# Kernel tuning notes

Measured on AMD Instinct MI355X. Metric: run time of the kernel, lower is better.

The kernel has to match this reference:

```python
import jax, jax.numpy as jnp
import numpy as np

B, N, C_IN, C_EMB, G = 16, 1024, 16, 64, 128
NEG = -1e12


def _lap(m):
    # m @ D^-1/2, transpose, @ D^-1/2  (matches torch code incl. transpose)
    d = jnp.sum(m, axis=1) ** -0.5
    return (m * d[None, :]).T * d[None, :]


def setup_inputs():
    key = jax.random.key(0)
    ks = jax.random.split(key, 16)
    f = jax.random.normal
    return {
        'x': f(ks[0], (B, C_IN, N), jnp.float32),
        'ct': f(ks[1], (B, C_EMB, N), jnp.float32),
        'graph_data': jax.random.uniform(ks[2], (2, N, N), dtype=jnp.float32),
        'emb_w': f(ks[3], (C_EMB, C_IN)) / np.sqrt(C_IN).astype(np.float32),
        'emb_b': f(ks[4], (C_EMB,)) * 0.01,
        'emb2_w': f(ks[5], (N, N)) / np.sqrt(N).astype(np.float32),
        'emb2_b': f(ks[6], (N,)) * 0.01,
        'att_W': f(ks[7], (C_EMB, C_EMB)) / np.sqrt(C_EMB).astype(np.float32),
        'att_a': f(ks[8], (2 * C_EMB, 1)) / np.sqrt(2 * C_EMB).astype(np.float32),
        'att_GL': f(ks[9], (N, G)) / np.sqrt(G).astype(np.float32),
        'uai_w': f(ks[10], (C_EMB, C_EMB)) / np.sqrt(C_EMB).astype(np.float32),
        'uai_b': f(ks[11], (C_EMB,)) * 0.01,
        'lin1_w': f(ks[12], (C_EMB, C_EMB)) / np.sqrt(C_EMB).astype(np.float32),
        'lin2_w': f(ks[13], (C_EMB, C_EMB)) / np.sqrt(C_EMB).astype(np.float32),
        'lin2_b': f(ks[14], (C_EMB,)) * 0.01,
        'ln_w': jnp.ones((C_EMB, N), jnp.float32),
        'ln_b': jnp.zeros((C_EMB, N), jnp.float32),
    }


def reference(x, ct, graph_data, emb_w, emb_b, emb2_w, emb2_b, att_W, att_a,
              att_GL, uai_w, uai_b, lin1_w, lin2_w, lin2_b, ln_w, ln_b):
    # emb: Conv1d k=1 -> leaky_relu -> Linear over node axis N
    h0 = jax.nn.leaky_relu(jnp.einsum('bcn,ec->ben', x, emb_w) + emb_b[None, :, None])
    h0 = jnp.einsum('ben,mn->bem', h0, emb2_w) + emb2_b[None, None, :]
    inp = jnp.swapaxes(h0, 1, 2)  # [B,N,C']

    # InterpositionAttention (repeat/cat factorized: e_ij = leakyrelu(a1.h_i + a2.h_j))
    eye = jnp.eye(N, dtype=x.dtype)
    adj_att = jax.nn.softmax(jax.nn.relu(att_GL @ att_GL.T), axis=-1) + eye
    h = inp @ att_W  # [B,N,C']
    e = jax.nn.leaky_relu((h @ att_a[:C_EMB]) + jnp.swapaxes(h @ att_a[C_EMB:], 1, 2))  # [B,N,N]
    att = jax.nn.softmax(jnp.where(adj_att > 0, e, NEG), axis=2)
    x_att = jnp.swapaxes(jax.nn.relu(att @ h), 1, 2)  # [B,C',N]

    # UAI module (eval mode: dropout off -> all MC samples equal -> sigma = 0)
    mu = jnp.swapaxes(x_att, 1, 2) @ uai_w.T + uai_b  # [B,N,C']
    x_uai = jnp.swapaxes(mu, 1, 2)  # [B,C',N]

    g1 = _lap(graph_data[0] + eye)
    g2 = _lap(graph_data[1] + eye)

    # learned adjacency from pairwise squared distances (cdist p=2, squared)
    xf = jnp.swapaxes(x_uai, 1, 2)  # [B,N,C']
    sq = jnp.sum(xf * xf, axis=-1)
    d2 = jnp.maximum(sq[:, :, None] + sq[:, None, :] - 2.0 * (xf @ jnp.swapaxes(xf, 1, 2)), 0.0)
    gl = jax.nn.softmax(jnp.exp(-d2 / (2.0 * C_EMB)) + eye, axis=-1)  # sigma^2 = emb_size

    def ln(z):  # LayerNorm over last two dims [C', N]
        m = jnp.mean(z, axis=(1, 2), keepdims=True)
        v = jnp.var(z, axis=(1, 2), keepdims=True)
        return (z - m) / jnp.sqrt(v + 1e-5) * ln_w + ln_b

    l1 = lambda z: jnp.einsum('oc,bcn->bon', lin1_w, z)
    l2 = lambda z: jnp.einsum('oc,bcn->bon', lin2_w, z) + lin2_b[None, :, None]

    x_new = ln(l1(x_uai) @ gl + l1(l1(x_uai) @ g1) @ g2)
    ft = jax.nn.gelu(ln(l2(x_uai) @ gl + l2(l2(x_uai) @ g1) @ g2), approximate=False)
    rt = ft  # rt is computed by the identical expression (dropout off)

    ct_new = ft * ct + x_new - ft * x_new
    ht = rt * jax.nn.elu(ct_new) + x_uai - rt * x_uai
    return (ht, ct_new)
```

## Files before the change

kernel.cpp:

```cpp
#include <hip/hip_runtime.h>
#include <math.h>

typedef unsigned short u16;
typedef __attribute__((ext_vector_type(8))) short short8;
typedef __attribute__((ext_vector_type(4))) float floatx4;

constexpr int BATCH = 16;
constexpr int NI = 1024;
constexpr int CE = 64;
constexpr int CI = 16;
constexpr long long NN2  = (long long)NI * NI;
constexpr long long BCN  = (long long)BATCH * CE * NI;
constexpr long long BNv  = (long long)BATCH * NI;
constexpr long long BNN  = (long long)BATCH * NI * NI;
constexpr long long S1 = (long long)CE * NI;
constexpr long long S2 = 2 * S1;

__device__ __forceinline__ float lrelu01(float x) { return x > 0.f ? x : 0.01f * x; }

__device__ __forceinline__ u16 f2bf(float f) {
  unsigned u = __builtin_bit_cast(unsigned, f);
  return (u16)((u + 0x7fffu + ((u >> 16) & 1u)) >> 16);
}
__device__ __forceinline__ float bf2f(u16 h) {
  unsigned u = ((unsigned)h) << 16;
  return __builtin_bit_cast(float, u);
}
__device__ __forceinline__ unsigned fkey(float f) {
  unsigned u = __builtin_bit_cast(unsigned, f);
  return (u & 0x80000000u) ? ~u : (u | 0x80000000u);
}
__device__ __forceinline__ float funkey(unsigned k) {
  unsigned u = (k & 0x80000000u) ? (k & 0x7fffffffu) : ~k;
  return __builtin_bit_cast(float, u);
}

template<int BM, int BN, int MODE>
__global__ __launch_bounds__(256) void mgemm(
    const u16* __restrict__ Ag, const u16* __restrict__ B1g, const u16* __restrict__ B2g,
    int K1, int K, int lda, int ldb, long long bsA, long long bsB1,
    float* __restrict__ Cf, u16* __restrict__ Cb, int ldc, long long bsC,
    const float* __restrict__ aux1, const float* __restrict__ aux2,
    const float* __restrict__ aux3, const float* __restrict__ aux4,
    float* __restrict__ Zout)
{
  constexpr int RM = BM / 2, RN = BN / 2, MI = RM / 16, NJ = RN / 16;
  __shared__ __align__(16) u16 As[BM * 64];
  __shared__ __align__(16) u16 Bs[BN * 64];
  __shared__ __align__(16) u16 xa[MODE == 13 ? 32 * 72 : 1];
  const int z = blockIdx.z;
  const int n0 = blockIdx.x * BN;
  const int r0 = blockIdx.y * BM;
  const u16* Ab = Ag + (long long)z * bsA + (long long)r0 * lda;
  const u16* Bb1 = B1g + (long long)z * bsB1 + (long long)n0 * ldb;
  const int tid = threadIdx.x;
  const int lane = tid & 63;
  const int wid = tid >> 6;
  const int wr = wid >> 1, wc = wid & 1;
  const int q = lane >> 4, mlow = lane & 15;

  floatx4 acc[MI][NJ] = {};
  float zp[(BM * 8) / 256] = {};

  for (int k0 = 0; k0 < K; k0 += 64) {
    if constexpr (MODE == 13) {
      const float* s1z = aux2 + (long long)z * NI;
      const float* s2z = aux3 + (long long)z * NI;
      const float mb = funkey(((const unsigned*)aux4)[z]);
#pragma unroll
      for (int s = 0; s < (BM * 8) / 256; s++) {
        int cid = tid + s * 256;
        int r = cid >> 3, craw = cid & 7;
        float s1r = s1z[r0 + r];
        float mr = lrelu01(s1r + mb);
        const float* sp = s2z + k0 + craw * 8;
        float4 sa = *(const float4*)sp;
        float4 sb = *(const float4*)(sp + 4);
        float p0 = __expf(lrelu01(s1r + sa.x) - mr);
        float p1 = __expf(lrelu01(s1r + sa.y) - mr);
        float p2 = __expf(lrelu01(s1r + sa.z) - mr);
        float p3 = __expf(lrelu01(s1r + sa.w) - mr);
        float p4 = __expf(lrelu01(s1r + sb.x) - mr);
        float p5 = __expf(lrelu01(s1r + sb.y) - mr);
        float p6 = __expf(lrelu01(s1r + sb.z) - mr);
        float p7 = __expf(lrelu01(s1r + sb.w) - mr);
        zp[s] += p0 + p1 + p2 + p3 + p4 + p5 + p6 + p7;
        uint4 v;
        v.x = (unsigned)f2bf(p0) | ((unsigned)f2bf(p1) << 16);
        v.y = (unsigned)f2bf(p2) | ((unsigned)f2bf(p3) << 16);
        v.z = (unsigned)f2bf(p4) | ((unsigned)f2bf(p5) << 16);
        v.w = (unsigned)f2bf(p6) | ((unsigned)f2bf(p7) << 16);
        *(uint4*)&As[(r * 8 + (craw ^ (r & 7))) * 8] = v;
      }
    } else {
      const u16* Asrc = Ab + k0;
#pragma unroll
      for (int s = 0; s < (BM * 8) / 256; s++) {
        int cid = tid + s * 256;
        int r = cid >> 3, craw = cid & 7;
        uint4 v = *(const uint4*)(Asrc + (long long)r * lda + craw * 8);
        *(uint4*)&As[(r * 8 + (craw ^ (r & 7))) * 8] = v;
      }
    }
    {
      const u16* Bsrc = (k0 < K1) ? (Bb1 + k0)
                                  : (B2g + (long long)n0 * ldb + (k0 - K1));
#pragma unroll
      for (int s = 0; s < (BN * 8) / 256; s++) {
        int cid = tid + s * 256;
        int r = cid >> 3, craw = cid & 7;
        uint4 v = *(const uint4*)(Bsrc + (long long)r * ldb + craw * 8);
        *(uint4*)&Bs[(r * 8 + (craw ^ (r & 7))) * 8] = v;
      }
    }
    __syncthreads();
#pragma unroll
    for (int kh = 0; kh < 2; kh++) {
      const int kc = kh * 4 + q;
      short8 afr[MI], bfr[NJ];
#pragma unroll
      for (int i = 0; i < MI; i++) {
        int row = wr * RM + i * 16 + mlow;
        afr[i] = *(const short8*)&As[(row * 8 + (kc ^ (row & 7))) * 8];
      }
#pragma unroll
      for (int j = 0; j < NJ; j++) {
        int row = wc * RN + j * 16 + mlow;
        bfr[j] = *(const short8*)&Bs[(row * 8 + (kc ^ (row & 7))) * 8];
      }
#pragma unroll
      for (int i = 0; i < MI; i++)
#pragma unroll
        for (int j = 0; j < NJ; j++)
          acc[i][j] = __builtin_amdgcn_mfma_f32_16x16x32_bf16(afr[i], bfr[j], acc[i][j], 0, 0, 0);
    }
    __syncthreads();
  }

  if constexpr (MODE == 3) {
    const float* sqb = aux1 + (long long)z * NI;
#pragma unroll
    for (int i = 0; i < MI; i++) {
#pragma unroll
      for (int rg = 0; rg < 4; rg++) {
        int r = r0 + wr * RM + i * 16 + q * 4 + rg;
        float sqi = sqb[r];
        float rsum = 0.f;
#pragma unroll
        for (int j = 0; j < NJ; j++) {
          int ncol = n0 + wc * RN + j * 16 + mlow;
          float d2 = fmaxf(sqi + sqb[ncol] - 2.f * acc[i][j][rg], 0.f);
          float w = __expf(__expf(-d2 * (1.f / 128.f)) + (r == ncol ? 1.f : 0.f) - 2.f);
          Cb[(long long)z * bsC + (long long)r * ldc + ncol] = f2bf(w);
          rsum += w;
        }
        rsum += __shfl_xor(rsum, 1);
        rsum += __shfl_xor(rsum, 2);
        rsum += __shfl_xor(rsum, 4);
        rsum += __shfl_xor(rsum, 8);
        if (mlow == 0) atomicAdd(&Zout[(long long)z * NI + r], rsum);
      }
    }
  } else if constexpr (MODE == 11) {
    float* sred = (float*)As;
#pragma unroll
    for (int i = 0; i < MI; i++) {
#pragma unroll
      for (int rg = 0; rg < 4; rg++) {
        int rloc = wr * RM + i * 16 + q * 4 + rg;
        int r = r0 + rloc;
        float rb = aux3[r];
        float ps1 = 0.f, ps2 = 0.f;
#pragma unroll
        for (int j = 0; j < NJ; j++) {
          int ncol = n0 + wc * RN + j * 16 + mlow;
          float v = acc[i][j][rg] + rb;
          Cb[(long long)z * bsC + (long long)r * ldc + ncol] = f2bf(v);
          ps1 = fmaf(v, aux1[ncol], ps1);
          ps2 = fmaf(v, aux2[ncol], ps2);
        }
        ps1 += __shfl_xor(ps1, 1); ps1 += __shfl_xor(ps1, 2);
        ps1 += __shfl_xor(ps1, 4); ps1 += __shfl_xor(ps1, 8);
        ps2 += __shfl_xor(ps2, 1); ps2 += __shfl_xor(ps2, 2);
        ps2 += __shfl_xor(ps2, 4); ps2 += __shfl_xor(ps2, 8);
        if (mlow == 0) { sred[rloc * 2 + wc] = ps1; sred[128 + rloc * 2 + wc] = ps2; }
      }
    }
    __syncthreads();
    if (tid < 64) {
      float v1 = sred[tid * 2] + sred[tid * 2 + 1];
      float v2 = sred[128 + tid * 2] + sred[128 + tid * 2 + 1];
      Cf[(long long)z * NI + r0 + tid] = v1;
      Zout[(long long)z * NI + r0 + tid] = v2;
      float mx = v2;
      for (int off = 1; off < 64; off <<= 1) mx = fmaxf(mx, __shfl_xor(mx, off));
      if (tid == 0) atomicMax((unsigned*)B2g + z, fkey(mx));
    }
  } else if constexpr (MODE == 13) {
    float* zred = (float*)xa;
    float* zinv = (float*)xa + 256;
    zred[(tid >> 3) * 8 + (tid & 7)] = zp[0];
    __syncthreads();
    if (tid < 32) {
      float sum = 0.f;
#pragma unroll
      for (int j = 0; j < 8; j++) sum += zred[tid * 8 + j];
      zinv[tid] = 1.f / sum;
    }
    __syncthreads();
    float zr[4];
#pragma unroll
    for (int rg = 0; rg < 4; rg++) zr[rg] = zinv[wr * 16 + q * 4 + rg];
    __syncthreads();
#pragma unroll
    for (int j = 0; j < NJ; j++) {
#pragma unroll
      for (int rg = 0; rg < 4; rg++) {
        int row = wr * 16 + q * 4 + rg;
        int col = wc * RN + j * 16 + mlow;
        float v = fmaxf(acc[0][j][rg] * zr[rg], 0.f);
        xa[row * 72 + col] = f2bf(v);
      }
    }
#pragma unroll
    for (int s = 0; s < 2; s++) {
      int cid = tid + s * 256;
      int r = cid >> 3, craw = cid & 7;
      *(uint4*)&Bs[(r * 8 + (craw ^ (r & 7))) * 8] =
          *(const uint4*)(B2g + r * 64 + craw * 8);
    }
    __syncthreads();
    floatx4 acc2[2] = {};
#pragma unroll
    for (int kh = 0; kh < 2; kh++) {
      const int kc = kh * 4 + q;
      short8 a2 = *(const short8*)&xa[(wr * 16 + mlow) * 72 + kc * 8];
#pragma unroll
      for (int j = 0; j < 2; j++) {
        int orow = wc * 32 + j * 16 + mlow;
        short8 b2 = *(const short8*)&Bs[(orow * 8 + (kc ^ (orow & 7))) * 8];
        acc2[j] = __builtin_amdgcn_mfma_f32_16x16x32_bf16(a2, b2, acc2[j], 0, 0, 0);
      }
    }
#pragma unroll
    for (int rg = 0; rg < 4; rg++) {
      int row = r0 + wr * 16 + q * 4 + rg;
      float sqp = 0.f;
#pragma unroll
      for (int j = 0; j < 2; j++) {
        int o = wc * 32 + j * 16 + mlow;
        float v = acc2[j][rg] + aux1[o];
        Cb[(long long)z * bsC + (long long)row * ldc + o] = f2bf(v);
        sqp = fmaf(v, v, sqp);
      }
      sqp += __shfl_xor(sqp, 1);
      sqp += __shfl_xor(sqp, 2);
      sqp += __shfl_xor(sqp, 4);
      sqp += __shfl_xor(sqp, 8);
      if (mlow == 0) atomicAdd(&Zout[(long long)z * NI + row], sqp);
    }
  } else if constexpr (MODE == 5) {
    float ts = 0.f, tss = 0.f;
#pragma unroll
    for (int i = 0; i < MI; i++) {
#pragma unroll
      for (int j = 0; j < NJ; j++) {
#pragma unroll
        for (int rg = 0; rg < 4; rg++) {
          int r = r0 + wr * RM + i * 16 + q * 4 + rg;
          int ncol = n0 + wc * RN + j * 16 + mlow;
          float v = acc[i][j][rg];
          v += aux3[r] * aux1[(long long)z * NI + ncol] + aux4[r] * aux2[ncol];
          Cf[(long long)z * bsC + (long long)r * ldc + ncol] = v;
          ts += v;
          tss = fmaf(v, v, tss);
        }
      }
    }
    float* red = (float*)As;
    red[tid] = ts; red[256 + tid] = tss;
    __syncthreads();
    for (int st = 128; st > 0; st >>= 1) {
      if (tid < st) { red[tid] += red[tid + st]; red[256 + tid] += red[256 + tid + st]; }
      __syncthreads();
    }
    if (tid == 0) {
      const int half = r0 >> 6;
      atomicAdd(&Zout[z * 2 + half], red[0]);
      atomicAdd(&Zout[32 + z * 2 + half], red[256]);
    }
  } else {
#pragma unroll
    for (int i = 0; i < MI; i++) {
#pragma unroll
      for (int j = 0; j < NJ; j++) {
#pragma unroll
        for (int rg = 0; rg < 4; rg++) {
          int r = r0 + wr * RM + i * 16 + q * 4 + rg;
          int ncol = n0 + wc * RN + j * 16 + mlow;
          float v = acc[i][j][rg];
          if constexpr (MODE == 4) {
            int blk = r >> 6, oo = r & 63;
            int drow = ((blk & 1) << 6) + oo;
            if (blk < 2) v = v / aux1[(long long)z * NI + ncol];
            Cb[(long long)z * bsC + (long long)drow * 2048 + (long long)(blk >> 1) * 1024 + ncol] =
                f2bf(v);
          } else {
            Cb[(long long)z * bsC + (long long)r * ldc + ncol] = f2bf(v);
          }
        }
      }
    }
  }
}

__global__ __launch_bounds__(256) void lap_rowsum(const float* __restrict__ gd,
                                                  float* __restrict__ dr)
{
  const int ki = blockIdx.x;
  const float* row = gd + (long long)ki * NI;
  float s = 0.f;
  for (int j = threadIdx.x; j < NI; j += 256) s += row[j];
  __shared__ float red[256];
  red[threadIdx.x] = s; __syncthreads();
  for (int st = 128; st > 0; st >>= 1) {
    if (threadIdx.x < st) red[threadIdx.x] += red[threadIdx.x + st];
    __syncthreads();
  }
  if (threadIdx.x == 0) dr[ki] = rsqrtf(red[0] + 1.f);
}

__global__ __launch_bounds__(256) void mega_prep(
    const float* __restrict__ l1w, const float* __restrict__ l2w,
    const float* __restrict__ l2b, const float* __restrict__ uaiw,
    const float* __restrict__ attW, const float* __restrict__ atta,
    u16* __restrict__ stack4, float* __restrict__ rb2ext, float* __restrict__ rl2ext,
    u16* __restrict__ uaiw_bf, u16* __restrict__ attwT_bf, float* __restrict__ w12,
    const float* __restrict__ emb2w, u16* __restrict__ emb2w_bf,
    const float* __restrict__ x, const float* __restrict__ ew,
    const float* __restrict__ eb, u16* __restrict__ h0a,
    const float* __restrict__ gd, const float* __restrict__ dsum,
    u16* __restrict__ g2t, u16* __restrict__ g1,
    float* __restrict__ cs1)
{
  __shared__ float sm[1088];
  const int bid = blockIdx.x;
  const int t = threadIdx.x;
  if (bid < 98) {
    const int gid = bid * 256 + t;
    if (gid < 4096) {
      stack4[gid] = f2bf(l1w[gid]);
    } else if (gid < 8192) {
      stack4[gid] = f2bf(l2w[gid - 4096]);
    } else if (gid < 12288) {
      int tt = gid - 8192, o = tt >> 6, m = tt & 63;
      float s = 0.f;
      for (int c = 0; c < 64; c++) s = fmaf(l1w[o * 64 + c], l1w[c * 64 + m], s);
      stack4[gid] = f2bf(s);
    } else if (gid < 16384) {
      int tt = gid - 12288, o = tt >> 6, m = tt & 63;
      float s = 0.f;
      for (int c = 0; c < 64; c++) s = fmaf(l2w[o * 64 + c], l2w[c * 64 + m], s);
      stack4[gid] = f2bf(s);
    } else if (gid < 16512) {
      int r = gid - 16384;
      rb2ext[r] = (r < 64) ? 0.f : l2b[r - 64];
    } else if (gid < 16640) {
      int r = gid - 16512;
      float v = 0.f;
      if (r >= 64) { int o = r - 64; for (int c = 0; c < 64; c++) v = fmaf(l2w[o * 64 + c], l2b[c], v); }
      rl2ext[r] = v;
    } else if (gid < 20736) {
      uaiw_bf[gid - 16640] = f2bf(uaiw[gid - 16640]);
    } else if (gid < 24832) {
      int idx = gid - 20736;
      int k = idx >> 6, e = idx & 63;
      attwT_bf[idx] = f2bf(attW[e * 64 + k]);
    } else if (gid < 24960) {
      int c = gid - 24832;
      int cc = c & 63, which = c >> 6;
      float s = 0.f;
      for (int k = 0; k < 64; k++) s = fmaf(attW[cc * 64 + k], atta[which * 64 + k], s);
      w12[c] = s;
    }
  } else if (bid < 4194) {
    const long long i = (long long)(bid - 98) * 256 + t;
    emb2w_bf[i] = f2bf(emb2w[i]);
  } else if (bid < 5218) {
    const int be = bid - 4194;
    const int b = be >> 6, e = be & 63;
    float* w = sm;
    if (t < CI) w[t] = ew[e * CI + t];
    __syncthreads();
    const float bias = eb[e];
    const float* xb = x + (long long)b * CI * NI;
    u16* outp = h0a + (long long)be * NI;
    for (int n = t; n < NI; n += 256) {
      float a = bias;
#pragma unroll
      for (int c = 0; c < CI; c++) a = fmaf(xb[c * NI + n], w[c], a);
      outp[n] = f2bf(lrelu01(a));
    }
  } else if (bid < 9314) {
    const long long idx = (long long)(bid - 5218) * 256 + t;
    const int m = (int)(idx >> 10), j = (int)(idx & 1023);
    const float* d = dsum + NI;
    float v = (gd[NN2 + idx] + (m == j ? 1.f : 0.f)) * d[m] * d[j];
    g2t[idx] = f2bf(v);
  } else if (bid < 10338) {
    const int sub = bid - 9314;
    const int bx = (sub & 31) * 32, by = (sub >> 5) * 32;
    const int lx = t & 31, ly = t >> 5;
    float* tile = sm;
    for (int yy = ly; yy < 32; yy += 8)
      tile[yy * 33 + lx] = gd[(long long)(by + yy) * NI + bx + lx];
    __syncthreads();
    for (int yy = ly; yy < 32; yy += 8) {
      const int i = bx + yy, j = by + lx;
      float v = (tile[lx * 33 + yy] + (i == j ? 1.f : 0.f)) * dsum[i] * dsum[j];
      g1[(long long)i * NI + j] = f2bf(v);
    }
  } else {
    const int n = bid - 10338;
    float s = 0.f;
    for (int i = t; i < NI; i += 256) s = fmaf(gd[(long long)n * NI + i], dsum[i], s);
    float* red = sm;
    red[t] = s; __syncthreads();
    for (int st = 128; st > 0; st >>= 1) {
      if (t < st) red[t] += red[t + st];
      __syncthreads();
    }
    if (t == 0) cs1[n] = dsum[n] * (red[0] + dsum[n]);
  }
}

__global__ __launch_bounds__(256) void csv2_kernel(const float* __restrict__ gd1,
                                                   const float* __restrict__ d,
                                                   const float* __restrict__ cs1,
                                                   float* __restrict__ cs2,
                                                   float* __restrict__ v2)
{
  const int m = blockIdx.x;
  float s = 0.f, sv = 0.f;
  for (int n = threadIdx.x; n < NI; n += 256) {
    float g = gd1[(long long)m * NI + n] * d[n];
    s += g;
    sv = fmaf(g, cs1[n], sv);
  }
  __shared__ float r1[256], r2[256];
  r1[threadIdx.x] = s; r2[threadIdx.x] = sv; __syncthreads();
  for (int st = 128; st > 0; st >>= 1) {
    if (threadIdx.x < st) { r1[threadIdx.x] += r1[threadIdx.x + st]; r2[threadIdx.x] += r2[threadIdx.x + st]; }
    __syncthreads();
  }
  if (threadIdx.x == 0) {
    cs2[m] = d[m] * (r1[0] + d[m]);
    v2[m] = d[m] * (r2[0] + d[m] * cs1[m]);
  }
}

__global__ __launch_bounds__(256) void cc_kernel(const u16* __restrict__ W,
                                                 const float* __restrict__ Zgl,
                                                 const float* __restrict__ cs2,
                                                 float* __restrict__ cc)
{
  const int b = blockIdx.y;
  const int wid = threadIdx.x >> 6, lane = threadIdx.x & 63;
  const int m = blockIdx.x * 4 + wid;
  const u16* row = W + (long long)b * NN2 + (long long)m * NI;
  const float* zz = Zgl + (long long)b * NI;
  float s = 0.f;
#pragma unroll
  for (int it = 0; it < 4; it++) {
    const int j0 = it * 256 + lane * 4;
    uint2 pk = *(const uint2*)(row + j0);
    float4 zv = *(const float4*)(zz + j0);
    s += bf2f((u16)(pk.x & 0xffff)) / zv.x + bf2f((u16)(pk.x >> 16)) / zv.y
       + bf2f((u16)(pk.y & 0xffff)) / zv.z + bf2f((u16)(pk.y >> 16)) / zv.w;
  }
  for (int off = 1; off < 64; off <<= 1) s += __shfl_xor(s, off);
  if (lane == 0) cc[(long long)b * NI + m] = s + cs2[m];
}

__global__ __launch_bounds__(256) void ln_final_t(const float* __restrict__ T,
                                                  const float* __restrict__ stats,
                                                  const float* __restrict__ lnw,
                                                  const float* __restrict__ lnb,
                                                  const float* __restrict__ ct,
                                                  const u16* __restrict__ xuT,
                                                  float* __restrict__ outp)
{
  __shared__ float xs[64 * 65];
  const int blk = blockIdx.x;
  const int b = blk >> 4;
  const int n0 = (blk & 15) << 6;
  const int t = threadIdx.x;
  const int tc = t & 63, tr = t >> 6;
#pragma unroll
  for (int i = 0; i < 16; i++) {
    int nn = i * 4 + tr;
    xs[tc * 65 + nn] = bf2f(xuT[((long long)b << 16) + (long long)(n0 + nn) * 64 + tc]);
  }
  __syncthreads();
  const float inv_n = 1.f / 65536.f;
  const float m0 = stats[b * 2] * inv_n;
  const float m1 = stats[b * 2 + 1] * inv_n;
  const float rs0 = rsqrtf(fmaxf(stats[32 + b * 2] * inv_n - m0 * m0, 0.f) + 1e-5f);
  const float rs1 = rsqrtf(fmaxf(stats[32 + b * 2 + 1] * inv_n - m1 * m1, 0.f) + 1e-5f);
#pragma unroll
  for (int j = 0; j < 16; j++) {
    const int c = j * 4 + tr;
    const int n = n0 + tc;
    const int rem = c * NI + n;
    const long long toff = (long long)b * S2 + rem;
    const float t0 = T[toff];
    const float t1 = T[toff + S1];
    const float w = lnw[rem], bb = lnb[rem];
    const float xn = (t0 - m0) * rs0 * w + bb;
    float ft = (t1 - m1) * rs1 * w + bb;
    ft = 0.5f * ft * (1.f + erff(ft * 0.70710678118654752f));
    const float u = xs[c * 65 + tc];
    const long long oidx = ((long long)b << 16) + rem;
    const float cn = fmaf(ft, ct[oidx] - xn, xn);
    const float el = cn > 0.f ? cn : expm1f(cn);
    outp[oidx] = fmaf(ft, el - u, u);
    outp[BCN + oidx] = cn;
  }
}

extern "C" void kernel_launch(void* const* d_in, const int* in_sizes, int n_in,
                              void* d_out, int out_size, void* d_ws, size_t ws_size,
                              hipStream_t stream)
{
  (void)in_sizes; (void)n_in; (void)out_size; (void)ws_size;
  const float* x      = (const float*)d_in[0];
  const float* ct     = (const float*)d_in[1];
  const float* gdata  = (const float*)d_in[2];
  const float* emb_w  = (const float*)d_in[3];
  const float* emb_b  = (const float*)d_in[4];
  const float* emb2_w = (const float*)d_in[5];
  const float* emb2_b = (const float*)d_in[6];
  const float* att_W  = (const float*)d_in[7];
  const float* att_a  = (const float*)d_in[8];
  const float* uai_w  = (const float*)d_in[10];
  const float* uai_b  = (const float*)d_in[11];
  const float* lin1_w = (const float*)d_in[12];
  const float* lin2_w = (const float*)d_in[13];
  const float* lin2_b = (const float*)d_in[14];
  const float* ln_w   = (const float*)d_in[15];
  const float* ln_b   = (const float*)d_in[16];
  float* outp = (float*)d_out;

  float* ws = (float*)d_ws;
  long long o = 0;
  auto af = [&](long long n) { float* p = ws + o; o += (n + 63) & ~63LL; return p; };
  auto au = [&](long long n) { return (u16*)af((n + 1) / 2); };

  float* Tacc    = af(S2 * BATCH);
  float* s1      = af(BNv);
  float* s2      = af(BNv);
  float* dsum    = af(2 * NI);
  float* cs1v    = af(NI);
  float* cs2v    = af(NI);
  float* v2v     = af(NI);
  float* ccv     = af(BNv);
  float* rb2ext  = af(128);
  float* rl2ext  = af(128);
  float* w12     = af(128);
  float* zeroreg = af(2 * BNv + 80);
  float* Zgl     = zeroreg;
  float* sqv     = zeroreg + BNv;
  float* stats   = zeroreg + 2 * BNv;
  unsigned* s2mU = (unsigned*)(stats + 64);
  u16* emb2w_bf  = au(NN2);
  u16* h0a_bf    = au(S1 * BATCH);
  u16* h0Tb      = au(S1 * BATCH);
  u16* hTb       = au(S1 * BATCH);
  u16* xuaiTb    = au(S1 * BATCH);
  u16* g1b       = au(NN2);
  u16* g2tb      = au(NN2);
  u16* G12b      = au(NN2);
  u16* Abig      = au((long long)BATCH * 128 * 2048);
  u16* stack4    = au(256 * 64);
  u16* uaiw_bf   = au(CE * CE);
  u16* attwT_bf  = au(CE * CE);
  u16* bigW      = au(BNN);

  hipMemsetAsync(zeroreg, 0, (2 * BNv + 80) * sizeof(float), stream);

  lap_rowsum<<<2 * NI, 256, 0, stream>>>(gdata, dsum);

  mega_prep<<<11362, 256, 0, stream>>>(
      lin1_w, lin2_w, lin2_b, uai_w, att_W, att_a,
      stack4, rb2ext, rl2ext, uaiw_bf, attwT_bf, w12,
      emb2_w, emb2w_bf, x, emb_w, emb_b, h0a_bf,
      gdata, dsum, g2tb, g1b, cs1v);

  csv2_kernel<<<NI, 256, 0, stream>>>(gdata + NN2, dsum + NI, cs1v, cs2v, v2v);

  mgemm<64, 64, 6><<<dim3(16, 16, 1), 256, 0, stream>>>(
      g2tb, g1b, nullptr, NI, NI, NI, NI, 0, 0,
      nullptr, G12b, NI, 0, nullptr, nullptr, nullptr, nullptr, nullptr);

  mgemm<64, 64, 11><<<dim3(1, 16, BATCH), 256, 0, stream>>>(
      emb2w_bf, h0a_bf, (const u16*)s2mU, NI, NI, NI, NI, 0, S1,
      s1, h0Tb, CE, S1, w12, w12 + 64, emb2_b, nullptr, s2);

  mgemm<64, 64, 6><<<dim3(16, 1, BATCH), 256, 0, stream>>>(
      attwT_bf, h0Tb, nullptr, CE, CE, CE, CE, 0, S1,
      nullptr, hTb, NI, S1, nullptr, nullptr, nullptr, nullptr, nullptr);

  mgemm<32, 64, 13><<<dim3(1, 32, BATCH), 256, 0, stream>>>(
      hTb, hTb, uaiw_bf, NI, NI, NI, NI, 0, S1,
      nullptr, xuaiTb, CE, S1, uai_b, s1, s2, (const float*)s2mU, sqv);

  mgemm<128, 128, 3><<<dim3(8, 8, BATCH), 256, 0, stream>>>(
      xuaiTb, xuaiTb, nullptr, CE, CE, CE, CE, S1, S1,
      nullptr, bigW, NI, NN2, sqv, nullptr, nullptr, nullptr, Zgl);

  cc_kernel<<<dim3(NI / 4, BATCH), 256, 0, stream>>>(bigW, Zgl, cs2v, ccv);

  mgemm<64, 64, 4><<<dim3(16, 4, BATCH), 256, 0, stream>>>(
      stack4, xuaiTb, nullptr, CE, CE, CE, CE, 0, S1,
      nullptr, Abig, 0, (long long)128 * 2048, Zgl, nullptr, nullptr, nullptr, nullptr);

  mgemm<64, 64, 5><<<dim3(16, 2, BATCH), 256, 0, stream>>>(
      Abig, bigW, G12b, NI, 2 * NI, 2048, NI, (long long)128 * 2048, NN2,
      Tacc, nullptr, NI, S2, ccv, v2v, rb2ext, rl2ext, stats);

  ln_final_t<<<256, 256, 0, stream>>>(Tacc, stats, ln_w, ln_b, ct, xuaiTb, outp);
}
```

Baseline: 257.2 us.

## Reassociate embedding and attention-weight GEMMs, emit transposed conv output directly

The attention weight is now applied to the small conv-1d output before the large node-axis Linear, so the big N x N GEMM produces h directly. A new epilogue mode folds the Linear bias through the column sums of the attention weight and computes the attention logit projections from att_a. The conv-1d prep now writes its output transposed with vectorized stores, and the G12 GEMM tile shape changes. This removes the intermediate h0T round trip. The new epilogue's reduction and indexing must match the old semantics exactly.

Result: no change. 259.3 us (+0.8%).

```diff
diff --git a/kernel.cpp b/kernel.cpp
--- a/kernel.cpp
+++ b/kernel.cpp
@@ -161,39 +161,33 @@
         if (mlow == 0) atomicAdd(&Zout[(long long)z * NI + r], rsum);
       }
     }
-  } else if constexpr (MODE == 11) {
+  } else if constexpr (MODE == 14) {
+    float ps1 = 0.f, ps2 = 0.f;
+#pragma unroll
+    for (int i = 0; i < MI; i++) {
+#pragma unroll
+      for (int rg = 0; rg < 4; rg++) {
+        int r = wr * RM + i * 16 + q * 4 + rg;
+        int ncol = n0 + wc * RN + mlow;
+        float v = acc[i][0][rg] + aux3[r] * aux1[ncol];
+        Cb[(long long)z * bsC + (long long)r * ldc + ncol] = f2bf(v);
+        ps1 = fmaf(v, aux2[r], ps1);
+        ps2 = fmaf(v, aux2[64 + r], ps2);
+      }
+    }
+    ps1 += __shfl_xor(ps1, 16); ps1 += __shfl_xor(ps1, 32);
+    ps2 += __shfl_xor(ps2, 16); ps2 += __shfl_xor(ps2, 32);
     float* sred = (float*)As;
-#pragma unroll
-    for (int i = 0; i < MI; i++) {
-#pragma unroll
-      for (int rg = 0; rg < 4; rg++) {
-        int rloc = wr * RM + i * 16 + q * 4 + rg;
-        int r = r0 + rloc;
-        float rb = aux3[r];
-        float ps1 = 0.f, ps2 = 0.f;
-#pragma unroll
-        for (int j = 0; j < NJ; j++) {
-          int ncol = n0 + wc * RN + j * 16 + mlow;
-          float v = acc[i][j][rg] + rb;
-          Cb[(long long)z * bsC + (long long)r * ldc + ncol] = f2bf(v);
-          ps1 = fmaf(v, aux1[ncol], ps1);
-          ps2 = fmaf(v, aux2[ncol], ps2);
-        }
-        ps1 += __shfl_xor(ps1, 1); ps1 += __shfl_xor(ps1, 2);
-        ps1 += __shfl_xor(ps1, 4); ps1 += __shfl_xor(ps1, 8);
-        ps2 += __shfl_xor(ps2, 1); ps2 += __shfl_xor(ps2, 2);
-        ps2 += __shfl_xor(ps2, 4); ps2 += __shfl_xor(ps2, 8);
-        if (mlow == 0) { sred[rloc * 2 + wc] = ps1; sred[128 + rloc * 2 + wc] = ps2; }
-      }
-    }
-    __syncthreads();
-    if (tid < 64) {
+    const int col = wc * RN + mlow;
+    if (q == 0) { sred[col * 2 + wr] = ps1; sred[64 + col * 2 + wr] = ps2; }
+    __syncthreads();
+    if (tid < 32) {
       float v1 = sred[tid * 2] + sred[tid * 2 + 1];
-      float v2 = sred[128 + tid * 2] + sred[128 + tid * 2 + 1];
-      Cf[(long long)z * NI + r0 + tid] = v1;
-      Zout[(long long)z * NI + r0 + tid] = v2;
+      float v2 = sred[64 + tid * 2] + sred[64 + tid * 2 + 1];
+      Cf[(long long)z * NI + n0 + tid] = v1;
+      Zout[(long long)z * NI + n0 + tid] = v2;
       float mx = v2;
-      for (int off = 1; off < 64; off <<= 1) mx = fmaxf(mx, __shfl_xor(mx, off));
+      for (int off = 1; off < 32; off <<= 1) mx = fmaxf(mx, __shfl_xor(mx, off));
       if (tid == 0) atomicMax((unsigned*)B2g + z, fkey(mx));
     }
   } else if constexpr (MODE == 13) {
@@ -333,17 +327,17 @@
 __global__ __launch_bounds__(256) void mega_prep(
     const float* __restrict__ l1w, const float* __restrict__ l2w,
     const float* __restrict__ l2b, const float* __restrict__ uaiw,
-    const float* __restrict__ attW, const float* __restrict__ atta,
+    const float* __restrict__ attW,
     u16* __restrict__ stack4, float* __restrict__ rb2ext, float* __restrict__ rl2ext,
-    u16* __restrict__ uaiw_bf, u16* __restrict__ attwT_bf, float* __restrict__ w12,
+    u16* __restrict__ uaiw_bf, u16* __restrict__ attwT_bf, float* __restrict__ wcs,
     const float* __restrict__ emb2w, u16* __restrict__ emb2w_bf,
     const float* __restrict__ x, const float* __restrict__ ew,
-    const float* __restrict__ eb, u16* __restrict__ h0a,
+    const float* __restrict__ eb, u16* __restrict__ h0aT,
     const float* __restrict__ gd, const float* __restrict__ dsum,
     u16* __restrict__ g2t, u16* __restrict__ g1,
     float* __restrict__ cs1)
 {
-  __shared__ float sm[1088];
+  __shared__ float sm[1092];
   const int bid = blockIdx.x;
   const int t = threadIdx.x;
   if (bid < 98) {
@@ -374,41 +368,52 @@
       uaiw_bf[gid - 16640] = f2bf(uaiw[gid - 16640]);
     } else if (gid < 24832) {
       int idx = gid - 20736;
-      int k = idx >> 6, e = idx & 63;
-      attwT_bf[idx] = f2bf(attW[e * 64 + k]);
-    } else if (gid < 24960) {
+      int c = idx >> 6, e = idx & 63;
+      attwT_bf[idx] = f2bf(attW[e * 64 + c]);
+    } else if (gid < 24896) {
       int c = gid - 24832;
-      int cc = c & 63, which = c >> 6;
       float s = 0.f;
-      for (int k = 0; k < 64; k++) s = fmaf(attW[cc * 64 + k], atta[which * 64 + k], s);
-      w12[c] = s;
+      for (int e = 0; e < 64; e++) s += attW[e * 64 + c];
+      wcs[c] = s;
     }
   } else if (bid < 4194) {
     const long long i = (long long)(bid - 98) * 256 + t;
     emb2w_bf[i] = f2bf(emb2w[i]);
-  } else if (bid < 5218) {
-    const int be = bid - 4194;
-    const int b = be >> 6, e = be & 63;
-    float* w = sm;
-    if (t < CI) w[t] = ew[e * CI + t];
-    __syncthreads();
-    const float bias = eb[e];
-    const float* xb = x + (long long)b * CI * NI;
-    u16* outp = h0a + (long long)be * NI;
-    for (int n = t; n < NI; n += 256) {
-      float a = bias;
-#pragma unroll
-      for (int c = 0; c < CI; c++) a = fmaf(xb[c * NI + n], w[c], a);
-      outp[n] = f2bf(lrelu01(a));
-    }
-  } else if (bid < 9314) {
-    const long long idx = (long long)(bid - 5218) * 256 + t;
+  } else if (bid < 4450) {
+    const int sub = bid - 4194;
+    const int b = sub >> 4;
+    const int nc = (sub & 15) * 64;
+    float* we = sm;
+    float* be = sm + 1024;
+    for (int i = t; i < 1024; i += 256) we[i] = ew[i];
+    if (t < 64) be[t] = eb[t];
+    __syncthreads();
+    const int n = nc + (t >> 2);
+    const int e0 = (t & 3) * 16;
+    const float* xb = x + (long long)b * CI * NI + n;
+    float xv[16];
+#pragma unroll
+    for (int c = 0; c < CI; c++) xv[c] = xb[(long long)c * NI];
+    u16 out16[16];
+#pragma unroll
+    for (int ee = 0; ee < 16; ee++) {
+      const int e = e0 + ee;
+      float a = be[e];
+#pragma unroll
+      for (int c = 0; c < CI; c++) a = fmaf(xv[c], we[e * 16 + c], a);
+      out16[ee] = f2bf(lrelu01(a));
+    }
+    u16* dst = h0aT + (long long)b * S1 + (long long)n * 64 + e0;
+    *(uint4*)dst = *(uint4*)out16;
+    *(uint4*)(dst + 8) = *(uint4*)(out16 + 8);
+  } else if (bid < 8546) {
+    const long long idx = (long long)(bid - 4450) * 256 + t;
     const int m = (int)(idx >> 10), j = (int)(idx & 1023);
     const float* d = dsum + NI;
     float v = (gd[NN2 + idx] + (m == j ? 1.f : 0.f)) * d[m] * d[j];
     g2t[idx] = f2bf(v);
-  } else if (bid < 10338) {
-    const int sub = bid - 9314;
+  } else if (bid < 9570) {
+    const int sub = bid - 8546;
     const int bx = (sub & 31) * 32, by = (sub >> 5) * 32;
     const int lx = t & 31, ly = t >> 5;
     float* tile = sm;
@@ -421,7 +426,7 @@
       g1[(long long)i * NI + j] = f2bf(v);
     }
   } else {
-    const int n = bid - 10338;
+    const int n = bid - 9570;
     float s = 0.f;
     for (int i = t; i < NI; i += 256) s = fmaf(gd[(long long)n * NI + i], dsum[i], s);
     float* red = sm;
@@ -566,15 +571,15 @@
   float* ccv     = af(BNv);
   float* rb2ext  = af(128);
   float* rl2ext  = af(128);
-  float* w12     = af(128);
+  float* wcs     = af(64);
   float* zeroreg = af(2 * BNv + 80);
   float* Zgl     = zeroreg;
   float* sqv     = zeroreg + BNv;
   float* stats   = zeroreg + 2 * BNv;
   unsigned* s2mU = (unsigned*)(stats + 64);
   u16* emb2w_bf  = au(NN2);
-  u16* h0a_bf    = au(S1 * BATCH);
-  u16* h0Tb      = au(S1 * BATCH);
+  u16* h0aTb     = au(S1 * BATCH);
+  u16* ybf       = au(S1 * BATCH);
   u16* hTb       = au(S1 * BATCH);
   u16* xuaiTb    = au(S1 * BATCH);
   u16* g1b       = au(NN2);
@@ -590,25 +595,25 @@
 
   lap_rowsum<<<2 * NI, 256, 0, stream>>>(gdata, dsum);
 
-  mega_prep<<<11362, 256, 0, stream>>>(
-      lin1_w, lin2_w, lin2_b, uai_w, att_W, att_a,
-      stack4, rb2ext, rl2ext, uaiw_bf, attwT_bf, w12,
-      emb2_w, emb2w_bf, x, emb_w, emb_b, h0a_bf,
+  mega_prep<<<10594, 256, 0, stream>>>(
+      lin1_w, lin2_w, lin2_b, uai_w, att_W,
+      stack4, rb2ext, rl2ext, uaiw_bf, attwT_bf, wcs,
+      emb2_w, emb2w_bf, x, emb_w, emb_b, h0aTb,
       gdata, dsum, g2tb, g1b, cs1v);
 
   csv2_kernel<<<NI, 256, 0, stream>>>(gdata + NN2, dsum + NI, cs1v, cs2v, v2v);
 
-  mgemm<64, 64, 6><<<dim3(16, 16, 1), 256, 0, stream>>>(
+  mgemm<32, 64, 6><<<dim3(16, 32, 1), 256, 0, stream>>>(
       g2tb, g1b, nullptr, NI, NI, NI, NI, 0, 0,
       nullptr, G12b, NI, 0, nullptr, nullptr, nullptr, nullptr, nullptr);
 
-  mgemm<64, 64, 11><<<dim3(1, 16, BATCH), 256, 0, stream>>>(
-      emb2w_bf, h0a_bf, (const u16*)s2mU, NI, NI, NI, NI, 0, S1,
-      s1, h0Tb, CE, S1, w12, w12 + 64, emb2_b, nullptr, s2);
-
   mgemm<64, 64, 6><<<dim3(16, 1, BATCH), 256, 0, stream>>>(
-      attwT_bf, h0Tb, nullptr, CE, CE, CE, CE, 0, S1,
-      nullptr, hTb, NI, S1, nullptr, nullptr, nullptr, nullptr, nullptr);
+      attwT_bf, h0aTb, nullptr, CE, CE, CE, CE, 0, S1,
+      nullptr, ybf, NI, S1, nullptr, nullptr, nullptr, nullptr, nullptr);
+
+  mgemm<64, 32, 14><<<dim3(32, 1, BATCH), 256, 0, stream>>>(
+      ybf, emb2w_bf, (const u16*)s2mU, NI, NI, NI, NI, S1, 0,
+      s1, hTb, NI, S1, emb2_b, att_a, wcs, nullptr, s2);
 
   mgemm<32, 64, 13><<<dim3(1, 32, BATCH), 256, 0, stream>>>(
       hTb, hTb, uaiw_bf, NI, NI, NI, NI, 0, S1,
```
